# Optimization experiments

Measured on AMD Instinct MI355X. Metric: run time of the kernel, lower is better.

The kernel has to match this reference:

```python
import jax, jax.numpy as jnp
import numpy as np

ALPHA = 0.2    # LeakyReLU negative slope (init arg alpha)
HEADS = 8
EPS = 1e-5     # LayerNorm eps


def setup_inputs() -> dict:
    key = jax.random.key(0)
    ks = jax.random.split(key, 16)
    B, S, D = 4, 1024, 256
    dh = D // HEADS  # 32
    x = jax.random.normal(ks[0], (B, S, D), jnp.float32)
    adj = (jax.random.uniform(ks[1], (B, S, S)) < 0.05).astype(jnp.float32)
    adj = jnp.maximum(adj, jnp.eye(S, dtype=jnp.float32)[None])

    def w(k, shape, fan):
        return jax.random.normal(k, shape, jnp.float32) * (fan ** -0.5)

    # GAT layer 0: in->hidden (concat heads)
    W0 = w(ks[2], (D, D), D); a_src0 = w(ks[3], (HEADS, dh), dh); a_dst0 = w(ks[4], (HEADS, dh), dh)
    # GAT layer 1: hidden->hidden (concat heads)
    W1 = w(ks[5], (D, D), D); a_src1 = w(ks[6], (HEADS, dh), dh); a_dst1 = w(ks[7], (HEADS, dh), dh)
    # GAT layer 2: hidden->out (mean over heads, head_dim = out_dim)
    W2 = w(ks[8], (D, HEADS * D), D); a_src2 = w(ks[9], (HEADS, D), D); a_dst2 = w(ks[10], (HEADS, D), D)
    # LayerNorm
    ln_g = jnp.ones((D,), jnp.float32); ln_b = jnp.zeros((D,), jnp.float32)
    # FFN: D -> 2D -> D
    ff_w1 = w(ks[11], (D, 2 * D), D); ff_b1 = jnp.zeros((2 * D,), jnp.float32)
    ff_w2 = w(ks[12], (2 * D, D), 2 * D); ff_b2 = jnp.zeros((D,), jnp.float32)
    return dict(adj=adj, x=x, W0=W0, a_src0=a_src0, a_dst0=a_dst0,
                W1=W1, a_src1=a_src1, a_dst1=a_dst1,
                W2=W2, a_src2=a_src2, a_dst2=a_dst2,
                ln_g=ln_g, ln_b=ln_b,
                ff_w1=ff_w1, ff_b1=ff_b1, ff_w2=ff_w2, ff_b2=ff_b2)


def _gat_layer(h, adj, W, a_src, a_dst, concat):
    B, S, _ = h.shape
    hp = jnp.einsum('bsi,io->bso', h, W).reshape(B, S, HEADS, -1)  # [B,S,H,dh]
    src = jnp.einsum('bshd,hd->bsh', hp, a_src)  # per-node source score
    dst = jnp.einsum('bshd,hd->bsh', hp, a_dst)  # per-node dest score
    # e[b,i,j,h] = LeakyReLU(src_i + dst_j), masked by adjacency
    e = jax.nn.leaky_relu(src[:, :, None, :] + dst[:, None, :, :], ALPHA)
    e = jnp.where(adj[..., None] > 0, e, jnp.float32(-1e9))
    attn = jax.nn.softmax(e, axis=2)  # softmax over neighbors j
    out = jnp.einsum('bijh,bjhd->bihd', attn, hp)
    return out.reshape(B, S, -1) if concat else out.mean(axis=2)


def reference(adj, x, W0, a_src0, a_dst0, W1, a_src1, a_dst1, W2, a_src2, a_dst2,
              ln_g, ln_b, ff_w1, ff_b1, ff_w2, ff_b2):
    # MultiAttentionGAT: 3 layers with residuals, ELU between layers
    h = jax.nn.elu(_gat_layer(x, adj, W0, a_src0, a_dst0, True) + x)
    h = jax.nn.elu(_gat_layer(h, adj, W1, a_src1, a_dst1, True) + h)
    h = _gat_layer(h, adj, W2, a_src2, a_dst2, False) + h
    # LayerNorm
    mu = h.mean(-1, keepdims=True)
    var = h.var(-1, keepdims=True)
    h = (h - mu) * jax.lax.rsqrt(var + EPS) * ln_g + ln_b
    # GELU FFN + residual
    ff = jnp.dot(jax.nn.gelu(jnp.dot(h, ff_w1) + ff_b1), ff_w2) + ff_b2
    return h + ff
```

## Files before the change

kernel.cpp:

```cpp
#include <hip/hip_runtime.h>
#include <hip/hip_bf16.h>

#define B_ 4
#define S_ 1024
#define D_ 256
#define H_ 8
#define LRELU_ALPHA 0.2f
#define MAXDEG 128

typedef __attribute__((ext_vector_type(8))) short short8;
typedef __attribute__((ext_vector_type(4))) float floatx4;

__device__ __forceinline__ float bf2f(unsigned short u) {
    union { unsigned int i; float f; } c; c.i = ((unsigned int)u) << 16; return c.f;
}
__device__ __forceinline__ unsigned short f2bf(float f) {
    union { float f; unsigned int u; } c; c.f = f;
    unsigned int r = (c.u + 0x7FFF + ((c.u >> 16) & 1)) >> 16;
    return (unsigned short)r;
}

__device__ void castT_body(const float* __restrict__ W, unsigned short* __restrict__ out,
                           int K, int N, int k0, int n0, float (*t)[33], int tid) {
    int tx = tid & 31, ty = tid >> 5;
#pragma unroll
    for (int i = 0; i < 4; ++i)
        t[ty + 8 * i][tx] = W[(size_t)(k0 + ty + 8 * i) * N + n0 + tx];
    __syncthreads();
#pragma unroll
    for (int i = 0; i < 4; ++i)
        out[(size_t)(n0 + ty + 8 * i) * K + k0 + tx] = f2bf(t[tx][ty + 8 * i]);
}

__global__ __launch_bounds__(256) void k_prep(
        const float* __restrict__ x, unsigned short* __restrict__ xb,
        const float* __restrict__ W0, unsigned short* __restrict__ W0t,
        const float* __restrict__ W1, unsigned short* __restrict__ W1t,
        const float* __restrict__ W2, unsigned short* __restrict__ W2t,
        const float* __restrict__ F1, unsigned short* __restrict__ F1t,
        const float* __restrict__ F2, unsigned short* __restrict__ F2t,
        const float* __restrict__ as2, const float* __restrict__ ad2,
        float* __restrict__ WS2, float* __restrict__ WD2,
        const float* __restrict__ adj, int* __restrict__ nbr, int* __restrict__ cnt) {
    __shared__ float t[32][33];
    __shared__ int c;
    int b = blockIdx.x, tid = threadIdx.x;
    if (b < 1024) {
        int i = b * 256 + tid;
        float4 v = ((const float4*)x)[i];
        ushort4 u; u.x = f2bf(v.x); u.y = f2bf(v.y); u.z = f2bf(v.z); u.w = f2bf(v.w);
        ((ushort4*)xb)[i] = u;
    } else if (b < 1088) {
        int i = b - 1024; castT_body(W0, W0t, 256, 256, (i & 7) * 32, (i >> 3) * 32, t, tid);
    } else if (b < 1152) {
        int i = b - 1088; castT_body(W1, W1t, 256, 256, (i & 7) * 32, (i >> 3) * 32, t, tid);
    } else if (b < 1664) {
        int i = b - 1152;
        int k0 = (i & 7) * 32, d0 = ((i >> 3) & 7) * 32, h = i >> 6;
        int tx = tid & 31, ty = tid >> 5;
#pragma unroll
        for (int q = 0; q < 4; ++q)
            t[ty + 8 * q][tx] = W2[(size_t)(k0 + ty + 8 * q) * 2048 + h * 256 + d0 + tx];
        __syncthreads();
#pragma unroll
        for (int q = 0; q < 4; ++q)
            W2t[(size_t)(d0 + ty + 8 * q) * 2048 + h * 256 + k0 + tx] = f2bf(t[tx][ty + 8 * q]);
    } else if (b < 1792) {
        int i = b - 1664; castT_body(F1, F1t, 256, 512, (i & 7) * 32, (i >> 3) * 32, t, tid);
    } else if (b < 1920) {
        int i = b - 1792; castT_body(F2, F2t, 512, 256, (i & 15) * 32, (i >> 4) * 32, t, tid);
    } else if (b < 2432) {
        int id = (b - 1920) * 4 + (tid >> 6);
        int h = id >> 8, k = id & 255;
        int lane = tid & 63;
        float4 w4 = *(const float4*)(W2 + (size_t)k * 2048 + h * 256 + lane * 4);
        float4 a4 = *(const float4*)(as2 + h * 256 + lane * 4);
        float4 d4 = *(const float4*)(ad2 + h * 256 + lane * 4);
        float s = w4.x * a4.x + w4.y * a4.y + w4.z * a4.z + w4.w * a4.w;
        float d = w4.x * d4.x + w4.y * d4.y + w4.z * d4.z + w4.w * d4.w;
#pragma unroll
        for (int o = 32; o; o >>= 1) { s += __shfl_xor(s, o); d += __shfl_xor(d, o); }
        if (lane == 0) { WS2[h * 256 + k] = s; WD2[h * 256 + k] = d; }
    } else {
        int row = b - 2432;
        if (tid == 0) c = 0;
        __syncthreads();
        float4 a4 = ((const float4*)(adj + (size_t)row * S_))[tid];
#pragma unroll
        for (int q = 0; q < 4; ++q) {
            float a = q == 0 ? a4.x : q == 1 ? a4.y : q == 2 ? a4.z : a4.w;
            if (a > 0.f) {
                int s = atomicAdd(&c, 1);
                if (s < MAXDEG) nbr[row * MAXDEG + s] = tid * 4 + q;
            }
        }
        __syncthreads();
        if (tid == 0) cnt[row] = c < MAXDEG ? c : MAXDEG;
    }
}

__global__ __launch_bounds__(256) void k_gemm_wide(const unsigned short* __restrict__ A,
        const unsigned short* __restrict__ Bt, float* __restrict__ P,
        int M, int N, int K, int Kc) {
    __shared__ unsigned short As[64][40];
    __shared__ unsigned short Bs[256][40];
    int tid = threadIdx.x;
    int bm = blockIdx.y * 64, bn = blockIdx.x * 256;
    int kbeg = blockIdx.z * Kc, kend = kbeg + Kc;
    int lane = tid & 63, wv = tid >> 6;
    int lrow = lane & 15, lq = lane >> 4;
    floatx4 acc[4][4] = {};
    int sm = tid >> 2, skq = (tid & 3) * 8;
    const unsigned short* Ap = A + (size_t)(bm + sm) * K + skq;
    const unsigned short* Bp0 = Bt + (size_t)(bn + sm) * K + skq;
    const unsigned short* Bp1 = Bp0 + (size_t)64 * K;
    const unsigned short* Bp2 = Bp0 + (size_t)128 * K;
    const unsigned short* Bp3 = Bp0 + (size_t)192 * K;
    short8 av  = *(const short8*)(Ap + kbeg);
    short8 bv0 = *(const short8*)(Bp0 + kbeg);
    short8 bv1 = *(const short8*)(Bp1 + kbeg);
    short8 bv2 = *(const short8*)(Bp2 + kbeg);
    short8 bv3 = *(const short8*)(Bp3 + kbeg);
    for (int k0 = kbeg; k0 < kend; k0 += 32) {
        *(short8*)&As[sm][skq]        = av;
        *(short8*)&Bs[sm][skq]        = bv0;
        *(short8*)&Bs[sm + 64][skq]   = bv1;
        *(short8*)&Bs[sm + 128][skq]  = bv2;
        *(short8*)&Bs[sm + 192][skq]  = bv3;
        __syncthreads();
        if (k0 + 32 < kend) {
            av  = *(const short8*)(Ap + k0 + 32);
            bv0 = *(const short8*)(Bp0 + k0 + 32);
            bv1 = *(const short8*)(Bp1 + k0 + 32);
            bv2 = *(const short8*)(Bp2 + k0 + 32);
            bv3 = *(const short8*)(Bp3 + k0 + 32);
        }
        short8 aF[4], bF[4];
#pragma unroll
        for (int mi = 0; mi < 4; ++mi)
            aF[mi] = *(const short8*)&As[mi * 16 + lrow][lq * 8];
#pragma unroll
        for (int ni = 0; ni < 4; ++ni)
            bF[ni] = *(const short8*)&Bs[wv * 64 + ni * 16 + lrow][lq * 8];
#pragma unroll
        for (int mi = 0; mi < 4; ++mi)
#pragma unroll
            for (int ni = 0; ni < 4; ++ni)
                acc[mi][ni] = __builtin_amdgcn_mfma_f32_16x16x32_bf16(aF[mi], bF[ni], acc[mi][ni], 0, 0, 0);
        __syncthreads();
    }
    float* out = P + (size_t)blockIdx.z * M * N;
#pragma unroll
    for (int mi = 0; mi < 4; ++mi)
#pragma unroll
        for (int ni = 0; ni < 4; ++ni)
#pragma unroll
            for (int r = 0; r < 4; ++r) {
                int grow = bm + mi * 16 + lq * 4 + r;
                int gcol = bn + wv * 64 + ni * 16 + lrow;
                out[(size_t)grow * N + gcol] = acc[mi][ni][r];
            }
}

template<int EPI>
__global__ __launch_bounds__(256) void k_gemm64(
        const unsigned short* __restrict__ A, const unsigned short* __restrict__ Bt,
        int N, int K,
        float* __restrict__ Pout, unsigned short* __restrict__ Ob,
        const float* __restrict__ p1, const float* __restrict__ p2,
        float* __restrict__ SRC, float* __restrict__ DST) {
    __shared__ unsigned short As[2][64][40];
    __shared__ unsigned short Bs[2][64][40];
    int tid = threadIdx.x;
    int bm = blockIdx.y * 64, bn = blockIdx.x * 64;
    int lane = tid & 63, wv = tid >> 6;
    int lrow = lane & 15, lq = lane >> 4;
    floatx4 acc[4] = {};
    int sm = tid >> 2, skq = (tid & 3) * 8;
    const unsigned short* Ap = A + (size_t)(bm + sm) * K + skq;
    const unsigned short* Bp = Bt + (size_t)(bn + sm) * K + skq;
    short8 av = *(const short8*)Ap;
    short8 bv = *(const short8*)Bp;
    *(short8*)&As[0][sm][skq] = av;
    *(short8*)&Bs[0][sm][skq] = bv;
    __syncthreads();
    int cur = 0;
    for (int k0 = 0; k0 < K; k0 += 32) {
        bool more = k0 + 32 < K;
        if (more) {
            av = *(const short8*)(Ap + k0 + 32);
            bv = *(const short8*)(Bp + k0 + 32);
        }
        short8 aF = *(const short8*)&As[cur][wv * 16 + lrow][lq * 8];
        short8 bF[4];
#pragma unroll
        for (int ni = 0; ni < 4; ++ni)
            bF[ni] = *(const short8*)&Bs[cur][ni * 16 + lrow][lq * 8];
#pragma unroll
        for (int ni = 0; ni < 4; ++ni)
            acc[ni] = __builtin_amdgcn_mfma_f32_16x16x32_bf16(aF, bF[ni], acc[ni], 0, 0, 0);
        if (more) {
            *(short8*)&As[cur ^ 1][sm][skq] = av;
            *(short8*)&Bs[cur ^ 1][sm][skq] = bv;
            __syncthreads();
            cur ^= 1;
        }
    }
    int row0 = bm + wv * 16 + lq * 4;
    if (EPI == 0) {
#pragma unroll
        for (int ni = 0; ni < 4; ++ni)
#pragma unroll
            for (int r = 0; r < 4; ++r)
                Ob[(size_t)(row0 + r) * N + bn + ni * 16 + lrow] = f2bf(acc[ni][r]);
        float asv[4], adv[4];
#pragma unroll
        for (int ni = 0; ni < 4; ++ni) {
            asv[ni] = p1[bn + ni * 16 + lrow];
            adv[ni] = p2[bn + ni * 16 + lrow];
        }
#pragma unroll
        for (int r = 0; r < 4; ++r) {
            float sA = acc[0][r] * asv[0] + acc[1][r] * asv[1];
            float sB = acc[2][r] * asv[2] + acc[3][r] * asv[3];
            float dA = acc[0][r] * adv[0] + acc[1][r] * adv[1];
            float dB = acc[2][r] * adv[2] + acc[3][r] * adv[3];
#pragma unroll
            for (int o = 8; o; o >>= 1) {
                sA += __shfl_xor(sA, o); sB += __shfl_xor(sB, o);
                dA += __shfl_xor(dA, o); dB += __shfl_xor(dB, o);
            }
            if (lrow == 0) {
                int h0 = bn >> 5;
                SRC[(row0 + r) * 8 + h0]     = sA;
                SRC[(row0 + r) * 8 + h0 + 1] = sB;
                DST[(row0 + r) * 8 + h0]     = dA;
                DST[(row0 + r) * 8 + h0 + 1] = dB;
            }
        }
    } else if (EPI == 2) {
#pragma unroll
        for (int ni = 0; ni < 4; ++ni) {
            int gcol = bn + ni * 16 + lrow;
            float bb = p1[gcol];
#pragma unroll
            for (int r = 0; r < 4; ++r) {
                float xx = acc[ni][r] + bb;
                float tt = tanhf(0.7978845608028654f * (xx + 0.044715f * xx * xx * xx));
                Ob[(size_t)(row0 + r) * N + gcol] = f2bf(0.5f * xx * (1.f + tt));
            }
        }
    } else if (EPI == 3) {
#pragma unroll
        for (int ni = 0; ni < 4; ++ni) {
            int gcol = bn + ni * 16 + lrow;
            float bb = p1[gcol];
#pragma unroll
            for (int r = 0; r < 4; ++r) {
                float res = p2[(size_t)(row0 + r) * 256 + gcol];
                Pout[(size_t)(row0 + r) * 256 + gcol] = acc[ni][r] + bb + res;
            }
        }
    }
}

__global__ __launch_bounds__(256) void k_attn_small_f(const unsigned short* __restrict__ hp,
        const float* __restrict__ src, const float* __restrict__ dst,
        const int* __restrict__ nbr, const int* __restrict__ cnts,
        const float* __restrict__ X, float* __restrict__ Hout,
        unsigned short* __restrict__ Hb,
        const float* __restrict__ WS2, const float* __restrict__ WD2,
        float* __restrict__ SRC2, float* __restrict__ DST2) {
    int tid = threadIdx.x;
    int half = tid >> 7;
    int sub = tid & 127;
    int row = blockIdx.x * 2 + half;
    int rb = row & ~(S_ - 1);
    __shared__ int nb[2][MAXDEG];
    __shared__ float ss[2][8];
    __shared__ float ew[2][MAXDEG * 9];
    __shared__ float pr[2][2][16];
    int cnt = cnts[row];
    for (int t = sub; t < cnt; t += 128) nb[half][t] = nbr[row * MAXDEG + t];
    if (sub < 8) ss[half][sub] = src[row * H_ + sub];
    __syncthreads();
    for (int idx = sub; idx < cnt * 8; idx += 128) {
        int n = idx >> 3, h = idx & 7;
        int j = nb[half][n];
        float e = ss[half][h] + dst[(rb + j) * H_ + h];
        ew[half][n * 9 + h] = e > 0.f ? e : LRELU_ALPHA * e;
    }
    __syncthreads();
    {
        int wv2 = sub >> 6, lane = sub & 63;
        int h = wv2 * 4 + (lane >> 4), s16 = lane & 15;
        float m = -1e30f;
        for (int n = s16; n < cnt; n += 16) m = fmaxf(m, ew[half][n * 9 + h]);
        for (int o = 8; o; o >>= 1) m = fmaxf(m, __shfl_xor(m, o));
        float s = 0.f;
        for (int n = s16; n < cnt; n += 16) {
            float v = __expf(ew[half][n * 9 + h] - m); ew[half][n * 9 + h] = v; s += v;
        }
        for (int o = 8; o; o >>= 1) s += __shfl_xor(s, o);
        float inv = s > 0.f ? 1.f / s : 0.f;
        for (int n = s16; n < cnt; n += 16) ew[half][n * 9 + h] *= inv;
    }
    __syncthreads();
    int d0 = sub * 2;
    int h = sub >> 4;
    const unsigned short* hpb = hp + (size_t)rb * 256 + d0;
    const float* ewr = ew[half];
    float aA0 = 0.f, aA1 = 0.f, aB0 = 0.f, aB1 = 0.f;
    float aC0 = 0.f, aC1 = 0.f, aD0 = 0.f, aD1 = 0.f;
    int n = 0;
    for (; n + 3 < cnt; n += 4) {
        int j0 = nb[half][n], j1 = nb[half][n + 1];
        int j2 = nb[half][n + 2], j3 = nb[half][n + 3];
        unsigned int p0 = *(const unsigned int*)(hpb + (size_t)j0 * 256);
        unsigned int p1 = *(const unsigned int*)(hpb + (size_t)j1 * 256);
        unsigned int p2 = *(const unsigned int*)(hpb + (size_t)j2 * 256);
        unsigned int p3 = *(const unsigned int*)(hpb + (size_t)j3 * 256);
        float w0 = ewr[n * 9 + h], w1 = ewr[(n + 1) * 9 + h];
        float w2 = ewr[(n + 2) * 9 + h], w3 = ewr[(n + 3) * 9 + h];
        aA0 += w0 * bf2f((unsigned short)p0); aA1 += w0 * bf2f((unsigned short)(p0 >> 16));
        aB0 += w1 * bf2f((unsigned short)p1); aB1 += w1 * bf2f((unsigned short)(p1 >> 16));
        aC0 += w2 * bf2f((unsigned short)p2); aC1 += w2 * bf2f((unsigned short)(p2 >> 16));
        aD0 += w3 * bf2f((unsigned short)p3); aD1 += w3 * bf2f((unsigned short)(p3 >> 16));
    }
    for (; n < cnt; ++n) {
        int j = nb[half][n];
        unsigned int p = *(const unsigned int*)(hpb + (size_t)j * 256);
        float w = ewr[n * 9 + h];
        aA0 += w * bf2f((unsigned short)p); aA1 += w * bf2f((unsigned short)(p >> 16));
    }
    float2 xv = *(const float2*)(X + (size_t)row * 256 + d0);
    float ov0 = (aA0 + aB0) + (aC0 + aD0) + xv.x;
    float ov1 = (aA1 + aB1) + (aC1 + aD1) + xv.y;
    ov0 = ov0 > 0.f ? ov0 : (__expf(ov0) - 1.f);
    ov1 = ov1 > 0.f ? ov1 : (__expf(ov1) - 1.f);
    *(float2*)(Hout + (size_t)row * 256 + d0) = make_float2(ov0, ov1);
    ushort2 ub; ub.x = f2bf(ov0); ub.y = f2bf(ov1);
    *(ushort2*)(Hb + (size_t)row * 256 + d0) = ub;
    if (WS2 != nullptr) {
        int wv2 = sub >> 6, lane = sub & 63;
#pragma unroll
        for (int hh = 0; hh < 8; ++hh) {
            float sP = ov0 * WS2[hh * 256 + d0] + ov1 * WS2[hh * 256 + d0 + 1];
            float dP = ov0 * WD2[hh * 256 + d0] + ov1 * WD2[hh * 256 + d0 + 1];
            for (int o = 32; o; o >>= 1) { sP += __shfl_xor(sP, o); dP += __shfl_xor(dP, o); }
            if (lane == 0) { pr[half][wv2][hh * 2] = sP; pr[half][wv2][hh * 2 + 1] = dP; }
        }
        __syncthreads();
        if (sub < 16) {
            float tv = pr[half][0][sub] + pr[half][1][sub];
            if ((sub & 1) == 0) SRC2[row * 8 + (sub >> 1)] = tv;
            else                DST2[row * 8 + (sub >> 1)] = tv;
        }
    }
}

__global__ __launch_bounds__(256) void k_attn_Y(const unsigned short* __restrict__ Hb,
        const float* __restrict__ src2, const float* __restrict__ dst2,
        const int* __restrict__ nbr, const int* __restrict__ cnts,
        unsigned short* __restrict__ Ycat) {
    int row = blockIdx.x;
    int tid = threadIdx.x;
    int rb = row & ~(S_ - 1);
    __shared__ int nb[MAXDEG];
    __shared__ float ss[8];
    __shared__ float ew[MAXDEG * 8];
    int cnt = cnts[row];
    for (int t = tid; t < cnt; t += 256) nb[t] = nbr[row * MAXDEG + t];
    if (tid < 8) ss[tid] = src2[row * H_ + tid];
    __syncthreads();
    for (int idx = tid; idx < cnt * 8; idx += 256) {
        int n = idx >> 3, h = idx & 7;
        int j = nb[n];
        float e = ss[h] + dst2[(rb + j) * H_ + h];
        ew[n * 8 + h] = e > 0.f ? e : LRELU_ALPHA * e;
    }
    __syncthreads();
    {
        int lane = tid & 63, wv = tid >> 6;
        int h = wv * 2 + (lane >> 5), sub = lane & 31;
        float m = -1e30f;
        for (int n = sub; n < cnt; n += 32) m = fmaxf(m, ew[n * 8 + h]);
        for (int o = 16; o; o >>= 1) m = fmaxf(m, __shfl_xor(m, o));
        float s = 0.f;
        for (int n = sub; n < cnt; n += 32) {
            float v = __expf(ew[n * 8 + h] - m); ew[n * 8 + h] = v; s += v;
        }
        for (int o = 16; o; o >>= 1) s += __shfl_xor(s, o);
        float inv = s > 0.f ? 0.125f / s : 0.f;
        for (int n = sub; n < cnt; n += 32) ew[n * 8 + h] *= inv;
    }
    __syncthreads();
    int dp = tid & 127, hg = tid >> 7;
    const unsigned short* hbase = Hb + (size_t)rb * 256 + 2 * dp;
    const float* ewh = ew + hg * 4;
    float a0x = 0.f, a0y = 0.f, a0z = 0.f, a0w = 0.f;
    float a1x = 0.f, a1y = 0.f, a1z = 0.f, a1w = 0.f;
    int n = 0;
    for (; n + 3 < cnt; n += 4) {
        int j0 = nb[n], j1 = nb[n + 1], j2 = nb[n + 2], j3 = nb[n + 3];
        unsigned int p0 = *(const unsigned int*)(hbase + (size_t)j0 * 256);
        unsigned int p1 = *(const unsigned int*)(hbase + (size_t)j1 * 256);
        unsigned int p2 = *(const unsigned int*)(hbase + (size_t)j2 * 256);
        unsigned int p3 = *(const unsigned int*)(hbase + (size_t)j3 * 256);
        float4 w0 = *(const float4*)(ewh + n * 8);
        float4 w1 = *(const float4*)(ewh + (n + 1) * 8);
        float4 w2 = *(const float4*)(ewh + (n + 2) * 8);
        float4 w3 = *(const float4*)(ewh + (n + 3) * 8);
        float v0a = bf2f((unsigned short)p0), v0b = bf2f((unsigned short)(p0 >> 16));
        float v1a = bf2f((unsigned short)p1), v1b = bf2f((unsigned short)(p1 >> 16));
        float v2a = bf2f((unsigned short)p2), v2b = bf2f((unsigned short)(p2 >> 16));
        float v3a = bf2f((unsigned short)p3), v3b = bf2f((unsigned short)(p3 >> 16));
        a0x += w0.x * v0a + w1.x * v1a + w2.x * v2a + w3.x * v3a;
        a0y += w0.y * v0a + w1.y * v1a + w2.y * v2a + w3.y * v3a;
        a0z += w0.z * v0a + w1.z * v1a + w2.z * v2a + w3.z * v3a;
        a0w += w0.w * v0a + w1.w * v1a + w2.w * v2a + w3.w * v3a;
        a1x += w0.x * v0b + w1.x * v1b + w2.x * v2b + w3.x * v3b;
        a1y += w0.y * v0b + w1.y * v1b + w2.y * v2b + w3.y * v3b;
        a1z += w0.z * v0b + w1.z * v1b + w2.z * v2b + w3.z * v3b;
        a1w += w0.w * v0b + w1.w * v1b + w2.w * v2b + w3.w * v3b;
    }
    for (; n < cnt; ++n) {
        int j = nb[n];
        unsigned int p = *(const unsigned int*)(hbase + (size_t)j * 256);
        float4 w = *(const float4*)(ewh + n * 8);
        float va = bf2f((unsigned short)p), vb = bf2f((unsigned short)(p >> 16));
        a0x += w.x * va; a0y += w.y * va; a0z += w.z * va; a0w += w.w * va;
        a1x += w.x * vb; a1y += w.y * vb; a1z += w.z * vb; a1w += w.w * vb;
    }
    unsigned short* yb = Ycat + (size_t)row * 2048 + (hg * 4) * 256 + 2 * dp;
    ushort2 u;
    u.x = f2bf(a0x); u.y = f2bf(a1x); *(ushort2*)(yb)         = u;
    u.x = f2bf(a0y); u.y = f2bf(a1y); *(ushort2*)(yb + 256)   = u;
    u.x = f2bf(a0z); u.y = f2bf(a1z); *(ushort2*)(yb + 512)   = u;
    u.x = f2bf(a0w); u.y = f2bf(a1w); *(ushort2*)(yb + 768)   = u;
}

__global__ __launch_bounds__(256) void k_ln_red(const float* __restrict__ P, int nsplit,
        const float* __restrict__ Hres, const float* __restrict__ g,
        const float* __restrict__ bta, float* __restrict__ HLN,
        unsigned short* __restrict__ HLNb) {
    int row = blockIdx.x * 4 + (threadIdx.x >> 6);
    int lane = threadIdx.x & 63;
    float4 v = ((const float4*)(Hres + (size_t)row * 256))[lane];
    for (int sp = 0; sp < nsplit; ++sp) {
        float4 p = ((const float4*)(P + (size_t)sp * 1048576 + (size_t)row * 256))[lane];
        v.x += p.x; v.y += p.y; v.z += p.z; v.w += p.w;
    }
    float s = v.x + v.y + v.z + v.w;
    float q = v.x * v.x + v.y * v.y + v.z * v.z + v.w * v.w;
    for (int o = 32; o; o >>= 1) { s += __shfl_xor(s, o); q += __shfl_xor(q, o); }
    float mu = s * (1.f / 256.f);
    float var = q * (1.f / 256.f) - mu * mu;
    if (var < 0.f) var = 0.f;
    float rs = rsqrtf(var + 1e-5f);
    float4 gg = ((const float4*)g)[lane];
    float4 bb = ((const float4*)bta)[lane];
    float4 o;
    o.x = (v.x - mu) * rs * gg.x + bb.x;
    o.y = (v.y - mu) * rs * gg.y + bb.y;
    o.z = (v.z - mu) * rs * gg.z + bb.z;
    o.w = (v.w - mu) * rs * gg.w + bb.w;
    ((float4*)(HLN + (size_t)row * 256))[lane] = o;
    ushort4 ob; ob.x = f2bf(o.x); ob.y = f2bf(o.y); ob.z = f2bf(o.z); ob.w = f2bf(o.w);
    ((ushort4*)(HLNb + (size_t)row * 256))[lane] = ob;
}

extern "C" void kernel_launch(void* const* d_in, const int* in_sizes, int n_in,
                              void* d_out, int out_size, void* d_ws, size_t ws_size,
                              hipStream_t stream) {
    const float* adj   = (const float*)d_in[0];
    const float* x     = (const float*)d_in[1];
    const float* W0    = (const float*)d_in[2];
    const float* as0   = (const float*)d_in[3];
    const float* ad0   = (const float*)d_in[4];
    const float* W1    = (const float*)d_in[5];
    const float* as1   = (const float*)d_in[6];
    const float* ad1   = (const float*)d_in[7];
    const float* W2    = (const float*)d_in[8];
    const float* as2   = (const float*)d_in[9];
    const float* ad2   = (const float*)d_in[10];
    const float* ln_g  = (const float*)d_in[11];
    const float* ln_b  = (const float*)d_in[12];
    const float* ff_w1 = (const float*)d_in[13];
    const float* ff_b1 = (const float*)d_in[14];
    const float* ff_w2 = (const float*)d_in[15];
    const float* ff_b2 = (const float*)d_in[16];

    float* ws = (float*)d_ws;
    float* H    = ws;
    float* HLN  = ws + 1048576;
    unsigned short* Ycat = (unsigned short*)(ws + 2097152);
    unsigned short* HPb  = (unsigned short*)(ws + 6291456);
    unsigned short* xb   = (unsigned short*)(ws + 6815744);
    unsigned short* Hb   = (unsigned short*)(ws + 7340032);
    unsigned short* HLNb = (unsigned short*)(ws + 7864320);
    unsigned short* MIDb = (unsigned short*)(ws + 8388608);
    unsigned short* W0t  = (unsigned short*)(ws + 9437184);
    unsigned short* W1t  = (unsigned short*)(ws + 9469952);
    unsigned short* W2t  = (unsigned short*)(ws + 9502720);
    unsigned short* F1t  = (unsigned short*)(ws + 9764864);
    unsigned short* F2t  = (unsigned short*)(ws + 9830400);
    float* WS2  = ws + 9895936;
    float* WD2  = ws + 9897984;
    float* SRC  = ws + 9900032;
    float* DST  = ws + 9932800;
    float* SRC2 = ws + 9965568;
    float* DST2 = ws + 9998336;
    int*   NBR  = (int*)(ws + 10031104);
    int*   CNT  = (int*)(ws + 10555392);
    float* PP   = ws + 12582912;

    k_prep<<<6528, 256, 0, stream>>>(x, xb, W0, W0t, W1, W1t, W2, W2t,
                                     ff_w1, F1t, ff_w2, F2t, as2, ad2, WS2, WD2,
                                     adj, NBR, CNT);

    k_gemm64<0><<<dim3(4, 64), 256, 0, stream>>>(xb, W0t, 256, 256,
                                                 nullptr, HPb, as0, ad0, SRC, DST);
    k_attn_small_f<<<2048, 256, 0, stream>>>(HPb, SRC, DST, NBR, CNT, x, H, Hb,
                                             nullptr, nullptr, nullptr, nullptr);

    k_gemm64<0><<<dim3(4, 64), 256, 0, stream>>>(Hb, W1t, 256, 256,
                                                 nullptr, HPb, as1, ad1, SRC, DST);
    k_attn_small_f<<<2048, 256, 0, stream>>>(HPb, SRC, DST, NBR, CNT, H, H, Hb,
                                             WS2, WD2, SRC2, DST2);

    k_attn_Y<<<4096, 256, 0, stream>>>(Hb, SRC2, DST2, NBR, CNT, Ycat);
    k_gemm_wide<<<dim3(1, 64, 8), 256, 0, stream>>>(Ycat, W2t, PP, 4096, 256, 2048, 256);
    k_ln_red<<<1024, 256, 0, stream>>>(PP, 8, H, ln_g, ln_b, HLN, HLNb);

    k_gemm64<2><<<dim3(8, 64), 256, 0, stream>>>(HLNb, F1t, 512, 256,
                                                 nullptr, MIDb, ff_b1, nullptr, nullptr, nullptr);
    k_gemm64<3><<<dim3(4, 64), 256, 0, stream>>>(MIDb, F2t, 256, 512,
                                                 (float*)d_out, nullptr, ff_b2, HLN, nullptr, nullptr);
}
```

Before: 215.5 us.

## Remap attention kernels to one wavefront per row and two rows per block

The GAT aggregation kernel for layers 0 and 1 now gives each destination row a single 64-lane wavefront that handles 4 features per lane with 8-byte gathers. This removes the block-wide __syncthreads barriers and the shared-memory partial sums for the fused layer-2 score projection, at the cost of more serial work per lane. The layer-2 Y kernel now processes two rows per block, with each thread accumulating all 8 heads for 2 features. That halves the grid and gives more work per thread, but raises register pressure.

```diff
diff --git a/kernel.cpp b/kernel.cpp
--- a/kernel.cpp
+++ b/kernel.cpp
@@ -264,7 +264,7 @@
     }
 }
 
-__global__ __launch_bounds__(256) void k_attn_small_f(const unsigned short* __restrict__ hp,
+__global__ __launch_bounds__(256) void k_attn4(const unsigned short* __restrict__ hp,
         const float* __restrict__ src, const float* __restrict__ dst,
         const int* __restrict__ nbr, const int* __restrict__ cnts,
         const float* __restrict__ X, float* __restrict__ Hout,
@@ -272,172 +272,177 @@
         const float* __restrict__ WS2, const float* __restrict__ WD2,
         float* __restrict__ SRC2, float* __restrict__ DST2) {
     int tid = threadIdx.x;
-    int half = tid >> 7;
-    int sub = tid & 127;
+    int rq = tid >> 6;
+    int lane = tid & 63;
+    int row = blockIdx.x * 4 + rq;
+    int rb = row & ~(S_ - 1);
+    __shared__ int nb[4][MAXDEG];
+    __shared__ float ss[4][8];
+    __shared__ float ew[4][MAXDEG * 9];
+    int cnt = cnts[row];
+    for (int t = lane; t < cnt; t += 64) nb[rq][t] = nbr[row * MAXDEG + t];
+    if (lane < 8) ss[rq][lane] = src[row * H_ + lane];
+    for (int idx = lane; idx < cnt * 8; idx += 64) {
+        int n = idx >> 3, h = idx & 7;
+        int j = nb[rq][n];
+        float e = ss[rq][h] + dst[(rb + j) * H_ + h];
+        ew[rq][n * 9 + h] = e > 0.f ? e : LRELU_ALPHA * e;
+    }
+    {
+        int h = lane >> 3, s8 = lane & 7;
+        float m = -1e30f;
+        for (int n = s8; n < cnt; n += 8) m = fmaxf(m, ew[rq][n * 9 + h]);
+#pragma unroll
+        for (int o = 4; o; o >>= 1) m = fmaxf(m, __shfl_xor(m, o));
+        float s = 0.f;
+        for (int n = s8; n < cnt; n += 8) {
+            float v = __expf(ew[rq][n * 9 + h] - m); ew[rq][n * 9 + h] = v; s += v;
+        }
+#pragma unroll
+        for (int o = 4; o; o >>= 1) s += __shfl_xor(s, o);
+        float inv = s > 0.f ? 1.f / s : 0.f;
+        for (int n = s8; n < cnt; n += 8) ew[rq][n * 9 + h] *= inv;
+    }
+    int d0 = lane * 4;
+    int h = lane >> 3;
+    const unsigned short* hpb = hp + (size_t)rb * 256 + d0;
+    const float* ewr = ew[rq];
+    float A0 = 0.f, A1 = 0.f, A2 = 0.f, A3 = 0.f;
+    float B0 = 0.f, B1 = 0.f, B2 = 0.f, B3 = 0.f;
+    int n = 0;
+    for (; n + 3 < cnt; n += 4) {
+        int j0 = nb[rq][n], j1 = nb[rq][n + 1];
+        int j2 = nb[rq][n + 2], j3 = nb[rq][n + 3];
+        uint2 p0 = *(const uint2*)(hpb + (size_t)j0 * 256);
+        uint2 p1 = *(const uint2*)(hpb + (size_t)j1 * 256);
+        uint2 p2 = *(const uint2*)(hpb + (size_t)j2 * 256);
+        uint2 p3 = *(const uint2*)(hpb + (size_t)j3 * 256);
+        float w0 = ewr[n * 9 + h], w1 = ewr[(n + 1) * 9 + h];
+        float w2 = ewr[(n + 2) * 9 + h], w3 = ewr[(n + 3) * 9 + h];
+        A0 += w0 * bf2f((unsigned short)p0.x); A1 += w0 * bf2f((unsigned short)(p0.x >> 16));
+        A2 += w0 * bf2f((unsigned short)p0.y); A3 += w0 * bf2f((unsigned short)(p0.y >> 16));
+        B0 += w1 * bf2f((unsigned short)p1.x); B1 += w1 * bf2f((unsigned short)(p1.x >> 16));
+        B2 += w1 * bf2f((unsigned short)p1.y); B3 += w1 * bf2f((unsigned short)(p1.y >> 16));
+        A0 += w2 * bf2f((unsigned short)p2.x); A1 += w2 * bf2f((unsigned short)(p2.x >> 16));
+        A2 += w2 * bf2f((unsigned short)p2.y); A3 += w2 * bf2f((unsigned short)(p2.y >> 16));
+        B0 += w3 * bf2f((unsigned short)p3.x); B1 += w3 * bf2f((unsigned short)(p3.x >> 16));
+        B2 += w3 * bf2f((unsigned short)p3.y); B3 += w3 * bf2f((unsigned short)(p3.y >> 16));
+    }
+    for (; n < cnt; ++n) {
+        int j = nb[rq][n];
+        uint2 p = *(const uint2*)(hpb + (size_t)j * 256);
+        float w = ewr[n * 9 + h];
+        A0 += w * bf2f((unsigned short)p.x); A1 += w * bf2f((unsigned short)(p.x >> 16));
+        A2 += w * bf2f((unsigned short)p.y); A3 += w * bf2f((unsigned short)(p.y >> 16));
+    }
+    float4 xv = *(const float4*)(X + (size_t)row * 256 + d0);
+    float ov0 = A0 + B0 + xv.x;
+    float ov1 = A1 + B1 + xv.y;
+    float ov2 = A2 + B2 + xv.z;
+    float ov3 = A3 + B3 + xv.w;
+    ov0 = ov0 > 0.f ? ov0 : (__expf(ov0) - 1.f);
+    ov1 = ov1 > 0.f ? ov1 : (__expf(ov1) - 1.f);
+    ov2 = ov2 > 0.f ? ov2 : (__expf(ov2) - 1.f);
+    ov3 = ov3 > 0.f ? ov3 : (__expf(ov3) - 1.f);
+    *(float4*)(Hout + (size_t)row * 256 + d0) = make_float4(ov0, ov1, ov2, ov3);
+    ushort4 ub; ub.x = f2bf(ov0); ub.y = f2bf(ov1); ub.z = f2bf(ov2); ub.w = f2bf(ov3);
+    *(ushort4*)(Hb + (size_t)row * 256 + d0) = ub;
+    if (WS2 != nullptr) {
+#pragma unroll
+        for (int hh = 0; hh < 8; ++hh) {
+            float4 wsv = *(const float4*)(WS2 + hh * 256 + d0);
+            float4 wdv = *(const float4*)(WD2 + hh * 256 + d0);
+            float sP = ov0 * wsv.x + ov1 * wsv.y + ov2 * wsv.z + ov3 * wsv.w;
+            float dP = ov0 * wdv.x + ov1 * wdv.y + ov2 * wdv.z + ov3 * wdv.w;
+#pragma unroll
+            for (int o = 32; o; o >>= 1) { sP += __shfl_xor(sP, o); dP += __shfl_xor(dP, o); }
+            if (lane == 0) { SRC2[row * 8 + hh] = sP; DST2[row * 8 + hh] = dP; }
+        }
+    }
+}
+
+__global__ __launch_bounds__(256) void k_attn_Y(const unsigned short* __restrict__ Hb,
+        const float* __restrict__ src2, const float* __restrict__ dst2,
+        const int* __restrict__ nbr, const int* __restrict__ cnts,
+        unsigned short* __restrict__ Ycat) {
+    int tid = threadIdx.x;
+    int half = tid >> 7, sub = tid & 127;
     int row = blockIdx.x * 2 + half;
     int rb = row & ~(S_ - 1);
     __shared__ int nb[2][MAXDEG];
     __shared__ float ss[2][8];
-    __shared__ float ew[2][MAXDEG * 9];
-    __shared__ float pr[2][2][16];
+    __shared__ float ew[2][MAXDEG * 8];
     int cnt = cnts[row];
     for (int t = sub; t < cnt; t += 128) nb[half][t] = nbr[row * MAXDEG + t];
-    if (sub < 8) ss[half][sub] = src[row * H_ + sub];
+    if (sub < 8) ss[half][sub] = src2[row * H_ + sub];
     __syncthreads();
     for (int idx = sub; idx < cnt * 8; idx += 128) {
         int n = idx >> 3, h = idx & 7;
         int j = nb[half][n];
-        float e = ss[half][h] + dst[(rb + j) * H_ + h];
-        ew[half][n * 9 + h] = e > 0.f ? e : LRELU_ALPHA * e;
+        float e = ss[half][h] + dst2[(rb + j) * H_ + h];
+        ew[half][n * 8 + h] = e > 0.f ? e : LRELU_ALPHA * e;
     }
     __syncthreads();
     {
-        int wv2 = sub >> 6, lane = sub & 63;
-        int h = wv2 * 4 + (lane >> 4), s16 = lane & 15;
+        int h = sub >> 4, s16 = sub & 15;
         float m = -1e30f;
-        for (int n = s16; n < cnt; n += 16) m = fmaxf(m, ew[half][n * 9 + h]);
+        for (int n = s16; n < cnt; n += 16) m = fmaxf(m, ew[half][n * 8 + h]);
+#pragma unroll
         for (int o = 8; o; o >>= 1) m = fmaxf(m, __shfl_xor(m, o));
         float s = 0.f;
         for (int n = s16; n < cnt; n += 16) {
-            float v = __expf(ew[half][n * 9 + h] - m); ew[half][n * 9 + h] = v; s += v;
-        }
+            float v = __expf(ew[half][n * 8 + h] - m); ew[half][n * 8 + h] = v; s += v;
+        }
+#pragma unroll
         for (int o = 8; o; o >>= 1) s += __shfl_xor(s, o);
-        float inv = s > 0.f ? 1.f / s : 0.f;
-        for (int n = s16; n < cnt; n += 16) ew[half][n * 9 + h] *= inv;
+        float inv = s > 0.f ? 0.125f / s : 0.f;
+        for (int n = s16; n < cnt; n += 16) ew[half][n * 8 + h] *= inv;
     }
     __syncthreads();
-    int d0 = sub * 2;
-    int h = sub >> 4;
-    const unsigned short* hpb = hp + (size_t)rb * 256 + d0;
-    const float* ewr = ew[half];
-    float aA0 = 0.f, aA1 = 0.f, aB0 = 0.f, aB1 = 0.f;
-    float aC0 = 0.f, aC1 = 0.f, aD0 = 0.f, aD1 = 0.f;
+    const unsigned short* hbase = Hb + (size_t)rb * 256 + 2 * sub;
+    const float* ewh = ew[half];
+    float aA[8] = {}, aB[8] = {};
     int n = 0;
-    for (; n + 3 < cnt; n += 4) {
+    for (; n + 1 < cnt; n += 2) {
         int j0 = nb[half][n], j1 = nb[half][n + 1];
-        int j2 = nb[half][n + 2], j3 = nb[half][n + 3];
-        unsigned int p0 = *(const unsigned int*)(hpb + (size_t)j0 * 256);
-        unsigned int p1 = *(const unsigned int*)(hpb + (size_t)j1 * 256);
-        unsigned int p2 = *(const unsigned int*)(hpb + (size_t)j2 * 256);
-        unsigned int p3 = *(const unsigned int*)(hpb + (size_t)j3 * 256);
-        float w0 = ewr[n * 9 + h], w1 = ewr[(n + 1) * 9 + h];
-        float w2 = ewr[(n + 2) * 9 + h], w3 = ewr[(n + 3) * 9 + h];
-        aA0 += w0 * bf2f((unsigned short)p0); aA1 += w0 * bf2f((unsigned short)(p0 >> 16));
-        aB0 += w1 * bf2f((unsigned short)p1); aB1 += w1 * bf2f((unsigned short)(p1 >> 16));
-        aC0 += w2 * bf2f((unsigned short)p2); aC1 += w2 * bf2f((unsigned short)(p2 >> 16));
-        aD0 += w3 * bf2f((unsigned short)p3); aD1 += w3 * bf2f((unsigned short)(p3 >> 16));
+        unsigned int p0 = *(const unsigned int*)(hbase + (size_t)j0 * 256);
+        unsigned int p1 = *(const unsigned int*)(hbase + (size_t)j1 * 256);
+        float4 w0a = *(const float4*)(ewh + n * 8);
+        float4 w0b = *(const float4*)(ewh + n * 8 + 4);
+        float4 w1a = *(const float4*)(ewh + (n + 1) * 8);
+        float4 w1b = *(const float4*)(ewh + (n + 1) * 8 + 4);
+        float v0a = bf2f((unsigned short)p0), v0b = bf2f((unsigned short)(p0 >> 16));
+        float v1a = bf2f((unsigned short)p1), v1b = bf2f((unsigned short)(p1 >> 16));
+        aA[0] += w0a.x * v0a + w1a.x * v1a;  aB[0] += w0a.x * v0b + w1a.x * v1b;
+        aA[1] += w0a.y * v0a + w1a.y * v1a;  aB[1] += w0a.y * v0b + w1a.y * v1b;
+        aA[2] += w0a.z * v0a + w1a.z * v1a;  aB[2] += w0a.z * v0b + w1a.z * v1b;
+        aA[3] += w0a.w * v0a + w1a.w * v1a;  aB[3] += w0a.w * v0b + w1a.w * v1b;
+        aA[4] += w0b.x * v0a + w1b.x * v1a;  aB[4] += w0b.x * v0b + w1b.x * v1b;
+        aA[5] += w0b.y * v0a + w1b.y * v1a;  aB[5] += w0b.y * v0b + w1b.y * v1b;
+        aA[6] += w0b.z * v0a + w1b.z * v1a;  aB[6] += w0b.z * v0b + w1b.z * v1b;
+        aA[7] += w0b.w * v0a + w1b.w * v1a;  aB[7] += w0b.w * v0b + w1b.w * v1b;
     }
     for (; n < cnt; ++n) {
         int j = nb[half][n];
-        unsigned int p = *(const unsigned int*)(hpb + (size_t)j * 256);
-        float w = ewr[n * 9 + h];
-        aA0 += w * bf2f((unsigned short)p); aA1 += w * bf2f((unsigned short)(p >> 16));
-    }
-    float2 xv = *(const float2*)(X + (size_t)row * 256 + d0);
-    float ov0 = (aA0 + aB0) + (aC0 + aD0) + xv.x;
-    float ov1 = (aA1 + aB1) + (aC1 + aD1) + xv.y;
-    ov0 = ov0 > 0.f ? ov0 : (__expf(ov0) - 1.f);
-    ov1 = ov1 > 0.f ? ov1 : (__expf(ov1) - 1.f);
-    *(float2*)(Hout + (size_t)row * 256 + d0) = make_float2(ov0, ov1);
-    ushort2 ub; ub.x = f2bf(ov0); ub.y = f2bf(ov1);
-    *(ushort2*)(Hb + (size_t)row * 256 + d0) = ub;
-    if (WS2 != nullptr) {
-        int wv2 = sub >> 6, lane = sub & 63;
-#pragma unroll
-        for (int hh = 0; hh < 8; ++hh) {
-            float sP = ov0 * WS2[hh * 256 + d0] + ov1 * WS2[hh * 256 + d0 + 1];
-            float dP = ov0 * WD2[hh * 256 + d0] + ov1 * WD2[hh * 256 + d0 + 1];
-            for (int o = 32; o; o >>= 1) { sP += __shfl_xor(sP, o); dP += __shfl_xor(dP, o); }
-            if (lane == 0) { pr[half][wv2][hh * 2] = sP; pr[half][wv2][hh * 2 + 1] = dP; }
-        }
-        __syncthreads();
-        if (sub < 16) {
-            float tv = pr[half][0][sub] + pr[half][1][sub];
-            if ((sub & 1) == 0) SRC2[row * 8 + (sub >> 1)] = tv;
-            else                DST2[row * 8 + (sub >> 1)] = tv;
-        }
-    }
-}
-
-__global__ __launch_bounds__(256) void k_attn_Y(const unsigned short* __restrict__ Hb,
-        const float* __restrict__ src2, const float* __restrict__ dst2,
-        const int* __restrict__ nbr, const int* __restrict__ cnts,
-        unsigned short* __restrict__ Ycat) {
-    int row = blockIdx.x;
-    int tid = threadIdx.x;
-    int rb = row & ~(S_ - 1);
-    __shared__ int nb[MAXDEG];
-    __shared__ float ss[8];
-    __shared__ float ew[MAXDEG * 8];
-    int cnt = cnts[row];
-    for (int t = tid; t < cnt; t += 256) nb[t] = nbr[row * MAXDEG + t];
-    if (tid < 8) ss[tid] = src2[row * H_ + tid];
-    __syncthreads();
-    for (int idx = tid; idx < cnt * 8; idx += 256) {
-        int n = idx >> 3, h = idx & 7;
-        int j = nb[n];
-        float e = ss[h] + dst2[(rb + j) * H_ + h];
-        ew[n * 8 + h] = e > 0.f ? e : LRELU_ALPHA * e;
-    }
-    __syncthreads();
-    {
-        int lane = tid & 63, wv = tid >> 6;
-        int h = wv * 2 + (lane >> 5), sub = lane & 31;
-        float m = -1e30f;
-        for (int n = sub; n < cnt; n += 32) m = fmaxf(m, ew[n * 8 + h]);
-        for (int o = 16; o; o >>= 1) m = fmaxf(m, __shfl_xor(m, o));
-        float s = 0.f;
-        for (int n = sub; n < cnt; n += 32) {
-            float v = __expf(ew[n * 8 + h] - m); ew[n * 8 + h] = v; s += v;
-        }
-        for (int o = 16; o; o >>= 1) s += __shfl_xor(s, o);
-        float inv = s > 0.f ? 0.125f / s : 0.f;
-        for (int n = sub; n < cnt; n += 32) ew[n * 8 + h] *= inv;
-    }
-    __syncthreads();
-    int dp = tid & 127, hg = tid >> 7;
-    const unsigned short* hbase = Hb + (size_t)rb * 256 + 2 * dp;
-    const float* ewh = ew + hg * 4;
-    float a0x = 0.f, a0y = 0.f, a0z = 0.f, a0w = 0.f;
-    float a1x = 0.f, a1y = 0.f, a1z = 0.f, a1w = 0.f;
-    int n = 0;
-    for (; n + 3 < cnt; n += 4) {
-        int j0 = nb[n], j1 = nb[n + 1], j2 = nb[n + 2], j3 = nb[n + 3];
-        unsigned int p0 = *(const unsigned int*)(hbase + (size_t)j0 * 256);
-        unsigned int p1 = *(const unsigned int*)(hbase + (size_t)j1 * 256);
-        unsigned int p2 = *(const unsigned int*)(hbase + (size_t)j2 * 256);
-        unsigned int p3 = *(const unsigned int*)(hbase + (size_t)j3 * 256);
-        float4 w0 = *(const float4*)(ewh + n * 8);
-        float4 w1 = *(const float4*)(ewh + (n + 1) * 8);
-        float4 w2 = *(const float4*)(ewh + (n + 2) * 8);
-        float4 w3 = *(const float4*)(ewh + (n + 3) * 8);
-        float v0a = bf2f((unsigned short)p0), v0b = bf2f((unsigned short)(p0 >> 16));
-        float v1a = bf2f((unsigned short)p1), v1b = bf2f((unsigned short)(p1 >> 16));
-        float v2a = bf2f((unsigned short)p2), v2b = bf2f((unsigned short)(p2 >> 16));
-        float v3a = bf2f((unsigned short)p3), v3b = bf2f((unsigned short)(p3 >> 16));
-        a0x += w0.x * v0a + w1.x * v1a + w2.x * v2a + w3.x * v3a;
-        a0y += w0.y * v0a + w1.y * v1a + w2.y * v2a + w3.y * v3a;
-        a0z += w0.z * v0a + w1.z * v1a + w2.z * v2a + w3.z * v3a;
-        a0w += w0.w * v0a + w1.w * v1a + w2.w * v2a + w3.w * v3a;
-        a1x += w0.x * v0b + w1.x * v1b + w2.x * v2b + w3.x * v3b;
-        a1y += w0.y * v0b + w1.y * v1b + w2.y * v2b + w3.y * v3b;
-        a1z += w0.z * v0b + w1.z * v1b + w2.z * v2b + w3.z * v3b;
-        a1w += w0.w * v0b + w1.w * v1b + w2.w * v2b + w3.w * v3b;
-    }
-    for (; n < cnt; ++n) {
-        int j = nb[n];
         unsigned int p = *(const unsigned int*)(hbase + (size_t)j * 256);
-        float4 w = *(const float4*)(ewh + n * 8);
+        float4 wa = *(const float4*)(ewh + n * 8);
+        float4 wb = *(const float4*)(ewh + n * 8 + 4);
         float va = bf2f((unsigned short)p), vb = bf2f((unsigned short)(p >> 16));
-        a0x += w.x * va; a0y += w.y * va; a0z += w.z * va; a0w += w.w * va;
-        a1x += w.x * vb; a1y += w.y * vb; a1z += w.z * vb; a1w += w.w * vb;
-    }
-    unsigned short* yb = Ycat + (size_t)row * 2048 + (hg * 4) * 256 + 2 * dp;
-    ushort2 u;
-    u.x = f2bf(a0x); u.y = f2bf(a1x); *(ushort2*)(yb)         = u;
-    u.x = f2bf(a0y); u.y = f2bf(a1y); *(ushort2*)(yb + 256)   = u;
-    u.x = f2bf(a0z); u.y = f2bf(a1z); *(ushort2*)(yb + 512)   = u;
-    u.x = f2bf(a0w); u.y = f2bf(a1w); *(ushort2*)(yb + 768)   = u;
+        aA[0] += wa.x * va; aB[0] += wa.x * vb;
+        aA[1] += wa.y * va; aB[1] += wa.y * vb;
+        aA[2] += wa.z * va; aB[2] += wa.z * vb;
+        aA[3] += wa.w * va; aB[3] += wa.w * vb;
+        aA[4] += wb.x * va; aB[4] += wb.x * vb;
+        aA[5] += wb.y * va; aB[5] += wb.y * vb;
+        aA[6] += wb.z * va; aB[6] += wb.z * vb;
+        aA[7] += wb.w * va; aB[7] += wb.w * vb;
+    }
+    unsigned short* yb = Ycat + (size_t)row * 2048 + 2 * sub;
+#pragma unroll
+    for (int hh = 0; hh < 8; ++hh) {
+        ushort2 u; u.x = f2bf(aA[hh]); u.y = f2bf(aB[hh]);
+        *(ushort2*)(yb + hh * 256) = u;
+    }
 }
 
 __global__ __launch_bounds__(256) void k_ln_red(const float* __restrict__ P, int nsplit,
@@ -521,15 +526,15 @@
 
     k_gemm64<0><<<dim3(4, 64), 256, 0, stream>>>(xb, W0t, 256, 256,
                                                  nullptr, HPb, as0, ad0, SRC, DST);
-    k_attn_small_f<<<2048, 256, 0, stream>>>(HPb, SRC, DST, NBR, CNT, x, H, Hb,
-                                             nullptr, nullptr, nullptr, nullptr);
+    k_attn4<<<1024, 256, 0, stream>>>(HPb, SRC, DST, NBR, CNT, x, H, Hb,
+                                      nullptr, nullptr, nullptr, nullptr);
 
     k_gemm64<0><<<dim3(4, 64), 256, 0, stream>>>(Hb, W1t, 256, 256,
                                                  nullptr, HPb, as1, ad1, SRC, DST);
-    k_attn_small_f<<<2048, 256, 0, stream>>>(HPb, SRC, DST, NBR, CNT, H, H, Hb,
-                                             WS2, WD2, SRC2, DST2);
-
-    k_attn_Y<<<4096, 256, 0, stream>>>(Hb, SRC2, DST2, NBR, CNT, Ycat);
+    k_attn4<<<1024, 256, 0, stream>>>(HPb, SRC, DST, NBR, CNT, H, H, Hb,
+                                      WS2, WD2, SRC2, DST2);
+
+    k_attn_Y<<<2048, 256, 0, stream>>>(Hb, SRC2, DST2, NBR, CNT, Ycat);
     k_gemm_wide<<<dim3(1, 64, 8), 256, 0, stream>>>(Ycat, W2t, PP, 4096, 256, 2048, 256);
     k_ln_red<<<1024, 256, 0, stream>>>(PP, 8, H, ln_g, ln_b, HLN, HLNb);
 
```

New measurement: 214.3 us. Within noise of the previous version (-0.6%).
